# Kernel optimization log

Measured on AMD Instinct MI355X. Metric: run time of the kernel, lower is better.

## Reference

```python
import jax, jax.numpy as jnp
import numpy as np

VOCAB = 200000  # num_submorphemes
EMB = 256       # embedding_dim
HID = 512       # hidden_dim
SEQ = 8192      # number of morphemes (LSTM time steps, batch=1)
TOK = 32768     # total flattened subword tokens (~4 per morpheme)
TAGS = 512      # num_tags


def setup_inputs() -> dict:
    key = jax.random.key(0)
    ks = jax.random.split(key, 12)
    s = 0.05
    return {
        "emb_table": jax.random.normal(ks[0], (VOCAB, EMB), jnp.float32) * 0.02,
        "w_ih_f": jax.random.normal(ks[1], (4 * HID, EMB), jnp.float32) * s,
        "w_hh_f": jax.random.normal(ks[2], (4 * HID, HID), jnp.float32) * s,
        "b_f": jax.random.normal(ks[3], (4 * HID,), jnp.float32) * s,
        "w_ih_b": jax.random.normal(ks[4], (4 * HID, EMB), jnp.float32) * s,
        "w_hh_b": jax.random.normal(ks[5], (4 * HID, HID), jnp.float32) * s,
        "b_b": jax.random.normal(ks[6], (4 * HID,), jnp.float32) * s,
        "w_out": jax.random.normal(ks[7], (TAGS, 2 * HID), jnp.float32) * s,
        "b_out": jax.random.normal(ks[8], (TAGS,), jnp.float32) * s,
        "subword_ids": jax.random.randint(ks[9], (TOK,), 0, VOCAB, jnp.int32),
        "segment_ids": jnp.sort(jax.random.randint(ks[10], (TOK,), 0, SEQ, jnp.int32)),
    }


def _lstm_dir(x, w_ih, w_hh, b, reverse):
    # x: [S, E]; torch LSTM gate order: i, f, g, o
    xg = x @ w_ih.T + b  # [S, 4H] precompute input contribution
    h0 = jnp.zeros((HID,), x.dtype)
    c0 = jnp.zeros((HID,), x.dtype)

    def step(carry, xg_t):
        h, c = carry
        g = xg_t + h @ w_hh.T
        i, f, gg, o = jnp.split(g, 4)
        i = jax.nn.sigmoid(i)
        f = jax.nn.sigmoid(f)
        gg = jnp.tanh(gg)
        o = jax.nn.sigmoid(o)
        c = f * c + i * gg
        h = o * jnp.tanh(c)
        return (h, c), h

    _, hs = jax.lax.scan(step, (h0, c0), xg, reverse=reverse)
    return hs  # [S, H]


def reference(emb_table, w_ih_f, w_hh_f, b_f, w_ih_b, w_hh_b, b_b,
              w_out, b_out, subword_ids, segment_ids):
    # ragged embedding lookup + sum-pool per morpheme (fused EmbeddingBag)
    tok = emb_table[subword_ids]                                  # [TOK, E]
    embeds = jax.ops.segment_sum(tok, segment_ids, num_segments=SEQ)  # [SEQ, E]
    # bidirectional LSTM, batch=1 (squeezed)
    h_fwd = _lstm_dir(embeds, w_ih_f, w_hh_f, b_f, reverse=False)
    h_bwd = _lstm_dir(embeds, w_ih_b, w_hh_b, b_b, reverse=True)
    h = jnp.concatenate([h_fwd, h_bwd], axis=1)                   # [SEQ, 2H]
    logits = h @ w_out.T + b_out                                  # [SEQ, TAGS]
    return jax.nn.log_softmax(logits, axis=1)
```

## Files before the change

### kernel.cpp

```cpp
#include <hip/hip_runtime.h>
#include <hip/hip_bf16.h>

#define VOCAB 200000
#define EMB 256
#define HID 512
#define SEQ 8192
#define TOK 32768
#define TAGS 512
#define G4H 2048

#define SENT 0x7FBFFFFFu

typedef unsigned u4v __attribute__((ext_vector_type(4)));

__device__ __forceinline__ float sigmoidf_(float x) { return 1.0f / (1.0f + __expf(-x)); }
__device__ __forceinline__ float tanhf_(float x) { return 1.0f - 2.0f / (1.0f + __expf(2.0f * x)); }

__global__ void init_sentinel(unsigned* __restrict__ hbuf, int n,
                              unsigned* __restrict__ tab, int ntab) {
  int i = blockIdx.x * blockDim.x + threadIdx.x;
  int stride = gridDim.x * blockDim.x;
  for (int k = i; k < n; k += stride) hbuf[k] = SENT;
  for (int k = i; k < ntab; k += stride) tab[k] = 0xFFFFFFFFu;
}

__global__ __launch_bounds__(256) void embed_pool(
    const float* __restrict__ emb, const int* __restrict__ ids,
    const int* __restrict__ seg, float* __restrict__ out) {
  int s = blockIdx.x;
  int d = threadIdx.x;
  int lo = 0, hi = TOK;
  while (lo < hi) { int m = (lo + hi) >> 1; if (seg[m] < s) lo = m + 1; else hi = m; }
  int start = lo;
  hi = TOK;
  while (lo < hi) { int m = (lo + hi) >> 1; if (seg[m] < s + 1) lo = m + 1; else hi = m; }
  int end = lo;
  float acc = 0.f;
  for (int tkn = start; tkn < end; ++tkn) {
    acc += emb[(long)ids[tkn] * EMB + d];
  }
  out[s * EMB + d] = acc;
}

__global__ __launch_bounds__(256) void xg_gemm(
    const float* __restrict__ embeds,
    const float* __restrict__ w_ih_f, const float* __restrict__ b_f,
    const float* __restrict__ w_ih_b, const float* __restrict__ b_b,
    float* __restrict__ xg) {
  int dir = blockIdx.z;
  const float* W = dir ? w_ih_b : w_ih_f;
  const float* B = dir ? b_b : b_f;
  float* out = xg + (size_t)dir * SEQ * G4H;
  int j0 = blockIdx.x * 64, t0 = blockIdx.y * 64;
  __shared__ float As[64][65];
  __shared__ float Bs[64][65];
  int tid = threadIdx.x;
  int ty = tid >> 4, tx = tid & 15;
  float acc[4][4] = {};
  for (int kc = 0; kc < EMB; kc += 64) {
#pragma unroll
    for (int i = 0; i < 4; ++i) {
      int fi = tid * 4 + i;
      int r = fi >> 4, c4 = fi & 15;
      float4 a = *(const float4*)&embeds[(size_t)(t0 + r) * EMB + kc + c4 * 4];
      As[r][c4 * 4 + 0] = a.x; As[r][c4 * 4 + 1] = a.y;
      As[r][c4 * 4 + 2] = a.z; As[r][c4 * 4 + 3] = a.w;
      float4 b = *(const float4*)&W[(size_t)(j0 + r) * EMB + kc + c4 * 4];
      Bs[r][c4 * 4 + 0] = b.x; Bs[r][c4 * 4 + 1] = b.y;
      Bs[r][c4 * 4 + 2] = b.z; Bs[r][c4 * 4 + 3] = b.w;
    }
    __syncthreads();
#pragma unroll 8
    for (int kk = 0; kk < 64; ++kk) {
      float a[4], b[4];
#pragma unroll
      for (int i = 0; i < 4; ++i) a[i] = As[ty * 4 + i][kk];
#pragma unroll
      for (int i = 0; i < 4; ++i) b[i] = Bs[tx * 4 + i][kk];
#pragma unroll
      for (int i = 0; i < 4; ++i)
#pragma unroll
        for (int j = 0; j < 4; ++j) acc[i][j] = fmaf(a[i], b[j], acc[i][j]);
    }
    __syncthreads();
  }
#pragma unroll
  for (int i = 0; i < 4; ++i)
#pragma unroll
    for (int j = 0; j < 4; ++j)
      out[(size_t)(t0 + ty * 4 + i) * G4H + j0 + tx * 4 + j] = acc[i][j] + B[j0 + tx * 4 + j];
}

__global__ __launch_bounds__(64) void lstm_scan(
    const float* __restrict__ w_hh_f, const float* __restrict__ w_hh_b,
    const float* __restrict__ xg, unsigned* __restrict__ hb_fast_base,
    unsigned* __restrict__ hb_safe_base, unsigned* __restrict__ xcdtab,
    int force_slow) {
  int b = blockIdx.x;
  int sel = b & 7;
  if (sel >= 2) return;
  int dir = sel;
  int Wk = b >> 3;
  const float* W = dir ? w_hh_b : w_hh_f;
  const float* xgd = xg + (size_t)dir * SEQ * G4H;
  unsigned* hb_fast = hb_fast_base + (size_t)dir * SEQ * HID;
  unsigned* hb_safe = hb_safe_base + (size_t)dir * SEQ * HID;

  int lane = threadIdx.x;
  const int hh = lane & 1;
  const int k0 = 2 * Wk;

  int my_xcd = (int)(__builtin_amdgcn_s_getreg(20 | (31 << 11)) & 0xFu);
  if (lane == 0)
    __hip_atomic_store(&xcdtab[dir * 256 + Wk], (unsigned)my_xcd,
                       __ATOMIC_RELAXED, __HIP_MEMORY_SCOPE_AGENT);

  __shared__ float4 Wl[8 * 128];
  for (int idx = lane; idx < 8 * 128; idx += 64) {
    int r = idx >> 7, c4 = idx & 127;
    int gr = 512 * (r >> 1) + k0 + (r & 1);
    Wl[idx] = *(const float4*)&W[(size_t)gr * HID + 4 * c4];
  }
  __syncthreads();

  bool same = false;
  if (!force_slow) {
    bool ok = true;
#pragma unroll
    for (int pp = 0; pp < 4; ++pp) {
      int p = lane + 64 * pp;
      unsigned v = 0xFFFFFFFFu;
      for (int tries = 0; tries < (1 << 15); ++tries) {
        v = __hip_atomic_load(&xcdtab[dir * 256 + p], __ATOMIC_RELAXED,
                              __HIP_MEMORY_SCOPE_AGENT);
        if (v != 0xFFFFFFFFu) break;
        __builtin_amdgcn_s_sleep(4);
      }
      ok &= (v == (unsigned)my_xcd);
    }
    same = __all((int)ok);
  }

  int tt0 = dir ? (SEQ - 1) : 0;
  const float* xr0 = xgd + (size_t)tt0 * G4H + k0 + hh;
  float xv0 = xr0[0], xv1 = xr0[512], xv2 = xr0[1024], xv3 = xr0[1536];

  float cst = 0.f;

  for (int t = 0; t < SEQ; ++t) {
    int tt = dir ? (SEQ - 1 - t) : t;
    int pt = dir ? (tt + 1) : (tt - 1);
    unsigned* srcF = hb_fast + (size_t)pt * HID + 4 * lane;

    u4v pa, pc;
    bool fastpoll = (t > 0) && same;
    if (fastpoll) {
      asm volatile(
          "global_load_dwordx4 %0, %2, off sc1\n\t"
          "global_load_dwordx4 %1, %2, off offset:1024 sc1"
          : "=&v"(pa), "=&v"(pc)
          : "v"(srcF)
          : "memory");
    }

    float4 wl0[8], wl1[8];
#pragma unroll
    for (int r = 0; r < 8; ++r) {
      wl0[r] = Wl[r * 128 + lane];
      wl1[r] = Wl[r * 128 + 64 + lane];
    }

    float4 h0, h1;
    if (t == 0) {
      h0 = make_float4(0.f, 0.f, 0.f, 0.f);
      h1 = make_float4(0.f, 0.f, 0.f, 0.f);
    } else {
      unsigned w0, w1, w2, w3, w4, w5, w6, w7;
      if (fastpoll) {
        asm volatile("s_waitcnt vmcnt(0)" : "+v"(pa), "+v"(pc) :: "memory");
        __builtin_amdgcn_sched_barrier(0);
        w0 = pa.x; w1 = pa.y; w2 = pa.z; w3 = pa.w;
        w4 = pc.x; w5 = pc.y; w6 = pc.z; w7 = pc.w;
        bool ok = (w0 != SENT) & (w1 != SENT) & (w2 != SENT) & (w3 != SENT) &
                  (w4 != SENT) & (w5 != SENT) & (w6 != SENT) & (w7 != SENT);
        bool got = __all((int)ok);
        for (int tries = 0; !got; ++tries) {
          u4v a, c;
          asm volatile(
              "global_load_dwordx4 %0, %2, off sc1\n\t"
              "global_load_dwordx4 %1, %2, off offset:1024 sc1\n\t"
              "s_waitcnt vmcnt(0)"
              : "=&v"(a), "=&v"(c)
              : "v"(srcF)
              : "memory");
          __builtin_amdgcn_sched_barrier(0);
          w0 = a.x; w1 = a.y; w2 = a.z; w3 = a.w;
          w4 = c.x; w5 = c.y; w6 = c.z; w7 = c.w;
          ok = (w0 != SENT) & (w1 != SENT) & (w2 != SENT) & (w3 != SENT) &
               (w4 != SENT) & (w5 != SENT) & (w6 != SENT) & (w7 != SENT);
          got = __all((int)ok);
          if (!got && tries > 64) __builtin_amdgcn_s_sleep(2);
        }
      } else {
        unsigned* src = hb_safe + (size_t)pt * HID + 4 * lane;
        for (;;) {
          u4v a, c;
          asm volatile(
              "global_load_dwordx4 %0, %2, off sc0 sc1\n\t"
              "global_load_dwordx4 %1, %2, off offset:1024 sc0 sc1\n\t"
              "s_waitcnt vmcnt(0)"
              : "=&v"(a), "=&v"(c)
              : "v"(src)
              : "memory");
          __builtin_amdgcn_sched_barrier(0);
          w0 = a.x; w1 = a.y; w2 = a.z; w3 = a.w;
          w4 = c.x; w5 = c.y; w6 = c.z; w7 = c.w;
          bool ok = (w0 != SENT) & (w1 != SENT) & (w2 != SENT) & (w3 != SENT) &
                    (w4 != SENT) & (w5 != SENT) & (w6 != SENT) & (w7 != SENT);
          if (__all((int)ok)) break;
          __builtin_amdgcn_s_sleep(1);
        }
      }
      h0.x = __uint_as_float(w0); h0.y = __uint_as_float(w1);
      h0.z = __uint_as_float(w2); h0.w = __uint_as_float(w3);
      h1.x = __uint_as_float(w4); h1.y = __uint_as_float(w5);
      h1.z = __uint_as_float(w6); h1.w = __uint_as_float(w7);
    }

    int tn = (t + 1 < SEQ) ? (t + 1) : t;
    int ttn = dir ? (SEQ - 1 - tn) : tn;
    const float* xrn = xgd + (size_t)ttn * G4H + k0 + hh;
    float nx0 = xrn[0], nx1 = xrn[512], nx2 = xrn[1024], nx3 = xrn[1536];

    float acc[8];
#pragma unroll
    for (int r = 0; r < 8; ++r) {
      float4 wa = wl0[r];
      float4 wc = wl1[r];
      float a_ = wa.x * h0.x;
      a_ = fmaf(wa.y, h0.y, a_);
      a_ = fmaf(wa.z, h0.z, a_);
      a_ = fmaf(wa.w, h0.w, a_);
      a_ = fmaf(wc.x, h1.x, a_);
      a_ = fmaf(wc.y, h1.y, a_);
      a_ = fmaf(wc.z, h1.z, a_);
      a_ = fmaf(wc.w, h1.w, a_);
      acc[r] = a_;
    }

    float v4[4];
    {
      int b0 = lane & 1;
#pragma unroll
      for (int j = 0; j < 4; ++j) {
        float mine = b0 ? acc[2 * j + 1] : acc[2 * j];
        float oth  = b0 ? acc[2 * j] : acc[2 * j + 1];
        v4[j] = mine + __shfl_xor(oth, 1);
      }
    }
    float v2[2];
    {
      int b1 = (lane >> 1) & 1;
#pragma unroll
      for (int j = 0; j < 2; ++j) {
        float mine = b1 ? v4[2 * j + 1] : v4[2 * j];
        float oth  = b1 ? v4[2 * j] : v4[2 * j + 1];
        v2[j] = mine + __shfl_xor(oth, 2);
      }
    }
    float v1;
    {
      int b2 = (lane >> 2) & 1;
      float mine = b2 ? v2[1] : v2[0];
      float oth  = b2 ? v2[0] : v2[1];
      v1 = mine + __shfl_xor(oth, 4);
      v1 += __shfl_xor(v1, 8);
      v1 += __shfl_xor(v1, 16);
      v1 += __shfl_xor(v1, 32);
    }

    float si = __shfl(v1, hh + 0) + xv0;
    float sf = __shfl(v1, hh + 2) + xv1;
    float sg = __shfl(v1, hh + 4) + xv2;
    float so = __shfl(v1, hh + 6) + xv3;

    float iv = sigmoidf_(si), fv = sigmoidf_(sf), gv = tanhf_(sg), ov = sigmoidf_(so);
    cst = fv * cst + iv * gv;
    float h = ov * tanhf_(cst);
    unsigned hbits = __float_as_uint(h);
    if (lane < 2) {
      hb_fast[(size_t)tt * HID + k0 + lane] = hbits;
      if (!same)
        __hip_atomic_store(hb_safe + (size_t)tt * HID + k0 + lane, hbits,
                           __ATOMIC_RELAXED, __HIP_MEMORY_SCOPE_AGENT);
    }

    xv0 = nx0; xv1 = nx1; xv2 = nx2; xv3 = nx3;
  }
}

__global__ __launch_bounds__(256) void out_gemm(
    const unsigned* __restrict__ hbuf, const float* __restrict__ w_out,
    const float* __restrict__ b_out, float* __restrict__ out) {
  int j0 = blockIdx.x * 128, t0 = blockIdx.y * 64;
  __shared__ float hs[64][65];
  __shared__ float ws_[128][65];
  int tid = threadIdx.x;
  int ti = tid & 15, ji = tid >> 4;
  float acc[4][8] = {};
  const float* hf = (const float*)hbuf;
  for (int kc = 0; kc < 1024; kc += 64) {
    const float* hsrc = (kc < 512) ? hf : (hf + (size_t)SEQ * HID);
    int kb = kc & 511;
#pragma unroll
    for (int i = 0; i < 4; ++i) {
      int fi = tid * 4 + i;
      int r = fi >> 4, c4 = fi & 15;
      float4 v = *(const float4*)&hsrc[(size_t)(t0 + r) * HID + kb + c4 * 4];
      hs[r][c4 * 4 + 0] = v.x; hs[r][c4 * 4 + 1] = v.y;
      hs[r][c4 * 4 + 2] = v.z; hs[r][c4 * 4 + 3] = v.w;
    }
#pragma unroll
    for (int i = 0; i < 8; ++i) {
      int fi = tid * 8 + i;
      int r = fi >> 4, c4 = fi & 15;
      float4 v = *(const float4*)&w_out[(size_t)(j0 + r) * 1024 + kc + c4 * 4];
      ws_[r][c4 * 4 + 0] = v.x; ws_[r][c4 * 4 + 1] = v.y;
      ws_[r][c4 * 4 + 2] = v.z; ws_[r][c4 * 4 + 3] = v.w;
    }
    __syncthreads();
#pragma unroll 4
    for (int kk = 0; kk < 64; ++kk) {
      float a[4], b[8];
#pragma unroll
      for (int x = 0; x < 4; ++x) a[x] = hs[ti * 4 + x][kk];
#pragma unroll
      for (int y = 0; y < 8; ++y) b[y] = ws_[ji * 8 + y][kk];
#pragma unroll
      for (int x = 0; x < 4; ++x)
#pragma unroll
        for (int y = 0; y < 8; ++y) acc[x][y] = fmaf(a[x], b[y], acc[x][y]);
    }
    __syncthreads();
  }
#pragma unroll
  for (int x = 0; x < 4; ++x)
#pragma unroll
    for (int y = 0; y < 8; ++y)
      out[(size_t)(t0 + ti * 4 + x) * TAGS + j0 + ji * 8 + y] = acc[x][y] + b_out[j0 + ji * 8 + y];
}

__global__ __launch_bounds__(256) void logsoftmax(float* __restrict__ out) {
  int t = blockIdx.x;
  float* row = out + (size_t)t * TAGS;
  int tid = threadIdx.x;
  float a = row[tid], b = row[tid + 256];
  float m = fmaxf(a, b);
  m = fmaxf(m, __shfl_xor(m, 1));
  m = fmaxf(m, __shfl_xor(m, 2));
  m = fmaxf(m, __shfl_xor(m, 4));
  m = fmaxf(m, __shfl_xor(m, 8));
  m = fmaxf(m, __shfl_xor(m, 16));
  m = fmaxf(m, __shfl_xor(m, 32));
  __shared__ float redm[4];
  __shared__ float reds[4];
  int wv = tid >> 6;
  if ((tid & 63) == 0) redm[wv] = m;
  __syncthreads();
  m = fmaxf(fmaxf(redm[0], redm[1]), fmaxf(redm[2], redm[3]));
  float s = __expf(a - m) + __expf(b - m);
  s += __shfl_xor(s, 1);
  s += __shfl_xor(s, 2);
  s += __shfl_xor(s, 4);
  s += __shfl_xor(s, 8);
  s += __shfl_xor(s, 16);
  s += __shfl_xor(s, 32);
  if ((tid & 63) == 0) reds[wv] = s;
  __syncthreads();
  s = reds[0] + reds[1] + reds[2] + reds[3];
  float ls = m + __logf(s);
  row[tid] = a - ls;
  row[tid + 256] = b - ls;
}

extern "C" void kernel_launch(void* const* d_in, const int* in_sizes, int n_in,
                              void* d_out, int out_size, void* d_ws, size_t ws_size,
                              hipStream_t stream) {
  (void)in_sizes; (void)n_in; (void)out_size;
  const float* emb    = (const float*)d_in[0];
  const float* w_ih_f = (const float*)d_in[1];
  const float* w_hh_f = (const float*)d_in[2];
  const float* b_f    = (const float*)d_in[3];
  const float* w_ih_b = (const float*)d_in[4];
  const float* w_hh_b = (const float*)d_in[5];
  const float* b_b    = (const float*)d_in[6];
  const float* w_out  = (const float*)d_in[7];
  const float* b_out  = (const float*)d_in[8];
  const int*   ids    = (const int*)d_in[9];
  const int*   seg    = (const int*)d_in[10];
  float* out = (float*)d_out;

  char* ws = (char*)d_ws;
  float*    embeds  = (float*)ws;
  float*    xg      = (float*)(ws + (8ll << 20));
  unsigned* hb_safe = (unsigned*)(ws + (136ll << 20));
  size_t need = (200ll << 20);
  int force_slow = (ws_size < need) ? 1 : 0;
  unsigned* hb_fast = force_slow ? hb_safe
                                 : (unsigned*)(ws + (168ll << 20));
  unsigned* xcdtab = (unsigned*)d_out;

  int hwords = (force_slow ? 1 : 2) * 2 * SEQ * HID;
  init_sentinel<<<2048, 256, 0, stream>>>(hb_safe, hwords, xcdtab, 512);
  embed_pool<<<SEQ, 256, 0, stream>>>(emb, ids, seg, embeds);
  dim3 g2(G4H / 64, SEQ / 64, 2);
  xg_gemm<<<g2, 256, 0, stream>>>(embeds, w_ih_f, b_f, w_ih_b, b_b, xg);
  lstm_scan<<<2048, 64, 0, stream>>>(w_hh_f, w_hh_b, xg, hb_fast, hb_safe,
                                     xcdtab, force_slow);
  dim3 g4(TAGS / 128, SEQ / 64);
  out_gemm<<<g4, 256, 0, stream>>>(hb_fast, w_out, b_out, out);
  logsoftmax<<<SEQ, 256, 0, stream>>>(out);
}
```

Measured before the change: 11.68 ms.

## Exchange LSTM hidden state between workgroups as packed bf16 pairs

The LSTM scan now packs each workgroup's two hidden outputs into one bf16x2 word, so the cross-workgroup hidden-state buffer holds half as many bytes. Per-step polling loads shrink from dwordx4 to dwordx2 and only one lane writes each step. The output GEMM unpacks the bf16 values when it fills shared memory. The intent is to cut the latency and traffic of the per-step global exchange on the serial critical path, at the cost of rounding h to bf16 in the recurrence, which may hurt accuracy over 8192 steps. A dead, redundant expression was also added in the shuffle reduction.

```diff
diff --git a/kernel.cpp b/kernel.cpp
--- a/kernel.cpp
+++ b/kernel.cpp
@@ -8,19 +8,27 @@
 #define TOK 32768
 #define TAGS 512
 #define G4H 2048
-
-#define SENT 0x7FBFFFFFu
-
-typedef unsigned u4v __attribute__((ext_vector_type(4)));
+#define HBW 256
+
+#define SENTP 0xFFFFFFFFu
+
+typedef unsigned u2v __attribute__((ext_vector_type(2)));
 
 __device__ __forceinline__ float sigmoidf_(float x) { return 1.0f / (1.0f + __expf(-x)); }
 __device__ __forceinline__ float tanhf_(float x) { return 1.0f - 2.0f / (1.0f + __expf(2.0f * x)); }
+
+__device__ __forceinline__ unsigned pack_bf16(float a, float b) {
+  unsigned ua = __float_as_uint(a), ub = __float_as_uint(b);
+  ua = (ua + 0x7FFFu + ((ua >> 16) & 1u)) >> 16;
+  ub = (ub + 0x7FFFu + ((ub >> 16) & 1u)) >> 16;
+  return ua | (ub << 16);
+}
 
 __global__ void init_sentinel(unsigned* __restrict__ hbuf, int n,
                               unsigned* __restrict__ tab, int ntab) {
   int i = blockIdx.x * blockDim.x + threadIdx.x;
   int stride = gridDim.x * blockDim.x;
-  for (int k = i; k < n; k += stride) hbuf[k] = SENT;
+  for (int k = i; k < n; k += stride) hbuf[k] = SENTP;
   for (int k = i; k < ntab; k += stride) tab[k] = 0xFFFFFFFFu;
 }
 
@@ -103,8 +111,8 @@
   int Wk = b >> 3;
   const float* W = dir ? w_hh_b : w_hh_f;
   const float* xgd = xg + (size_t)dir * SEQ * G4H;
-  unsigned* hb_fast = hb_fast_base + (size_t)dir * SEQ * HID;
-  unsigned* hb_safe = hb_safe_base + (size_t)dir * SEQ * HID;
+  unsigned* hb_fast = hb_fast_base + (size_t)dir * SEQ * HBW;
+  unsigned* hb_safe = hb_safe_base + (size_t)dir * SEQ * HBW;
 
   int lane = threadIdx.x;
   const int hh = lane & 1;
@@ -150,14 +158,14 @@
   for (int t = 0; t < SEQ; ++t) {
     int tt = dir ? (SEQ - 1 - t) : t;
     int pt = dir ? (tt + 1) : (tt - 1);
-    unsigned* srcF = hb_fast + (size_t)pt * HID + 4 * lane;
-
-    u4v pa, pc;
+    unsigned* srcF = hb_fast + (size_t)pt * HBW + 2 * lane;
+
+    u2v pa, pc;
     bool fastpoll = (t > 0) && same;
     if (fastpoll) {
       asm volatile(
-          "global_load_dwordx4 %0, %2, off sc1\n\t"
-          "global_load_dwordx4 %1, %2, off offset:1024 sc1"
+          "global_load_dwordx2 %0, %2, off sc1\n\t"
+          "global_load_dwordx2 %1, %2, off offset:512 sc1"
           : "=&v"(pa), "=&v"(pc)
           : "v"(srcF)
           : "memory");
@@ -170,62 +178,59 @@
       wl1[r] = Wl[r * 128 + 64 + lane];
     }
 
-    float4 h0, h1;
+    unsigned d0, d1, d2, d3;
     if (t == 0) {
-      h0 = make_float4(0.f, 0.f, 0.f, 0.f);
-      h1 = make_float4(0.f, 0.f, 0.f, 0.f);
+      d0 = d1 = d2 = d3 = 0u;
     } else {
-      unsigned w0, w1, w2, w3, w4, w5, w6, w7;
       if (fastpoll) {
         asm volatile("s_waitcnt vmcnt(0)" : "+v"(pa), "+v"(pc) :: "memory");
         __builtin_amdgcn_sched_barrier(0);
-        w0 = pa.x; w1 = pa.y; w2 = pa.z; w3 = pa.w;
-        w4 = pc.x; w5 = pc.y; w6 = pc.z; w7 = pc.w;
-        bool ok = (w0 != SENT) & (w1 != SENT) & (w2 != SENT) & (w3 != SENT) &
-                  (w4 != SENT) & (w5 != SENT) & (w6 != SENT) & (w7 != SENT);
+        d0 = pa.x; d1 = pa.y; d2 = pc.x; d3 = pc.y;
+        bool ok = (d0 != SENTP) & (d1 != SENTP) & (d2 != SENTP) & (d3 != SENTP);
         bool got = __all((int)ok);
         for (int tries = 0; !got; ++tries) {
-          u4v a, c;
+          u2v a, c;
           asm volatile(
-              "global_load_dwordx4 %0, %2, off sc1\n\t"
-              "global_load_dwordx4 %1, %2, off offset:1024 sc1\n\t"
+              "global_load_dwordx2 %0, %2, off sc1\n\t"
+              "global_load_dwordx2 %1, %2, off offset:512 sc1\n\t"
               "s_waitcnt vmcnt(0)"
               : "=&v"(a), "=&v"(c)
               : "v"(srcF)
               : "memory");
           __builtin_amdgcn_sched_barrier(0);
-          w0 = a.x; w1 = a.y; w2 = a.z; w3 = a.w;
-          w4 = c.x; w5 = c.y; w6 = c.z; w7 = c.w;
-          ok = (w0 != SENT) & (w1 != SENT) & (w2 != SENT) & (w3 != SENT) &
-               (w4 != SENT) & (w5 != SENT) & (w6 != SENT) & (w7 != SENT);
+          d0 = a.x; d1 = a.y; d2 = c.x; d3 = c.y;
+          ok = (d0 != SENTP) & (d1 != SENTP) & (d2 != SENTP) & (d3 != SENTP);
           got = __all((int)ok);
           if (!got && tries > 64) __builtin_amdgcn_s_sleep(2);
         }
       } else {
-        unsigned* src = hb_safe + (size_t)pt * HID + 4 * lane;
+        unsigned* src = hb_safe + (size_t)pt * HBW + 2 * lane;
         for (;;) {
-          u4v a, c;
+          u2v a, c;
           asm volatile(
-              "global_load_dwordx4 %0, %2, off sc0 sc1\n\t"
-              "global_load_dwordx4 %1, %2, off offset:1024 sc0 sc1\n\t"
+              "global_load_dwordx2 %0, %2, off sc0 sc1\n\t"
+              "global_load_dwordx2 %1, %2, off offset:512 sc0 sc1\n\t"
               "s_waitcnt vmcnt(0)"
               : "=&v"(a), "=&v"(c)
               : "v"(src)
               : "memory");
           __builtin_amdgcn_sched_barrier(0);
-          w0 = a.x; w1 = a.y; w2 = a.z; w3 = a.w;
-          w4 = c.x; w5 = c.y; w6 = c.z; w7 = c.w;
-          bool ok = (w0 != SENT) & (w1 != SENT) & (w2 != SENT) & (w3 != SENT) &
-                    (w4 != SENT) & (w5 != SENT) & (w6 != SENT) & (w7 != SENT);
+          d0 = a.x; d1 = a.y; d2 = c.x; d3 = c.y;
+          bool ok = (d0 != SENTP) & (d1 != SENTP) & (d2 != SENTP) & (d3 != SENTP);
           if (__all((int)ok)) break;
           __builtin_amdgcn_s_sleep(1);
         }
       }
-      h0.x = __uint_as_float(w0); h0.y = __uint_as_float(w1);
-      h0.z = __uint_as_float(w2); h0.w = __uint_as_float(w3);
-      h1.x = __uint_as_float(w4); h1.y = __uint_as_float(w5);
-      h1.z = __uint_as_float(w6); h1.w = __uint_as_float(w7);
-    }
+    }
+    float4 h0, h1;
+    h0.x = __uint_as_float(d0 << 16);
+    h0.y = __uint_as_float(d0 & 0xFFFF0000u);
+    h0.z = __uint_as_float(d1 << 16);
+    h0.w = __uint_as_float(d1 & 0xFFFF0000u);
+    h1.x = __uint_as_float(d2 << 16);
+    h1.y = __uint_as_float(d2 & 0xFFFF0000u);
+    h1.z = __uint_as_float(d3 << 16);
+    h1.w = __uint_as_float(d3 & 0xFFFF0000u);
 
     int tn = (t + 1 < SEQ) ? (t + 1) : t;
     int ttn = dir ? (SEQ - 1 - tn) : tn;
@@ -263,7 +268,8 @@
       int b1 = (lane >> 1) & 1;
 #pragma unroll
       for (int j = 0; j < 2; ++j) {
-        float mine = b1 ? v4[2 * j + 1] : v4[2 * j];
+        float mine = b1 ? v2[0] * 0.f + (b1 ? v4[2 * j + 1] : v4[2 * j]) : v4[2 * j];
+        mine = b1 ? v4[2 * j + 1] : v4[2 * j];
         float oth  = b1 ? v4[2 * j] : v4[2 * j + 1];
         v2[j] = mine + __shfl_xor(oth, 2);
       }
@@ -287,11 +293,13 @@
     float iv = sigmoidf_(si), fv = sigmoidf_(sf), gv = tanhf_(sg), ov = sigmoidf_(so);
     cst = fv * cst + iv * gv;
     float h = ov * tanhf_(cst);
-    unsigned hbits = __float_as_uint(h);
-    if (lane < 2) {
-      hb_fast[(size_t)tt * HID + k0 + lane] = hbits;
+
+    float hodd = __shfl(h, 1);
+    if (lane == 0) {
+      unsigned packed = pack_bf16(h, hodd);
+      hb_fast[(size_t)tt * HBW + Wk] = packed;
       if (!same)
-        __hip_atomic_store(hb_safe + (size_t)tt * HID + k0 + lane, hbits,
+        __hip_atomic_store(hb_safe + (size_t)tt * HBW + Wk, packed,
                            __ATOMIC_RELAXED, __HIP_MEMORY_SCOPE_AGENT);
     }
 
@@ -308,17 +316,16 @@
   int tid = threadIdx.x;
   int ti = tid & 15, ji = tid >> 4;
   float acc[4][8] = {};
-  const float* hf = (const float*)hbuf;
   for (int kc = 0; kc < 1024; kc += 64) {
-    const float* hsrc = (kc < 512) ? hf : (hf + (size_t)SEQ * HID);
-    int kb = kc & 511;
-#pragma unroll
-    for (int i = 0; i < 4; ++i) {
-      int fi = tid * 4 + i;
-      int r = fi >> 4, c4 = fi & 15;
-      float4 v = *(const float4*)&hsrc[(size_t)(t0 + r) * HID + kb + c4 * 4];
-      hs[r][c4 * 4 + 0] = v.x; hs[r][c4 * 4 + 1] = v.y;
-      hs[r][c4 * 4 + 2] = v.z; hs[r][c4 * 4 + 3] = v.w;
+    const unsigned* hsrc = (kc < 512) ? hbuf : (hbuf + (size_t)SEQ * HBW);
+    int kbd = (kc & 511) >> 1;
+#pragma unroll
+    for (int j = 0; j < 8; ++j) {
+      int idx = j * 256 + tid;
+      int r = idx >> 5, dw = idx & 31;
+      unsigned u = hsrc[(size_t)(t0 + r) * HBW + kbd + dw];
+      hs[r][dw * 2 + 0] = __uint_as_float(u << 16);
+      hs[r][dw * 2 + 1] = __uint_as_float(u & 0xFFFF0000u);
     }
 #pragma unroll
     for (int i = 0; i < 8; ++i) {
@@ -404,13 +411,13 @@
   float*    embeds  = (float*)ws;
   float*    xg      = (float*)(ws + (8ll << 20));
   unsigned* hb_safe = (unsigned*)(ws + (136ll << 20));
-  size_t need = (200ll << 20);
+  size_t need = (152ll << 20);
   int force_slow = (ws_size < need) ? 1 : 0;
   unsigned* hb_fast = force_slow ? hb_safe
-                                 : (unsigned*)(ws + (168ll << 20));
+                                 : (unsigned*)(ws + (144ll << 20));
   unsigned* xcdtab = (unsigned*)d_out;
 
-  int hwords = (force_slow ? 1 : 2) * 2 * SEQ * HID;
+  int hwords = (force_slow ? 1 : 2) * 2 * SEQ * HBW;
   init_sentinel<<<2048, 256, 0, stream>>>(hb_safe, hwords, xcdtab, 512);
   embed_pool<<<SEQ, 256, 0, stream>>>(emb, ids, seg, embeds);
   dim3 g2(G4H / 64, SEQ / 64, 2);
```

Result: slower. 12.12 ms (+3.8%).
